# Optimization experiments

Hardware: AMD Instinct MI355X
Metric: run time of the kernel (lower is better)

## Reference

```python
import jax, jax.numpy as jnp
import numpy as np

B = 262144   # number of (group, item) prediction pairs
M = 16       # max members per group (ragged -> padded)
NU = 100000  # num_users
NI = 50000   # num_items
D = 32       # embedding_dim (hardcoded via torch.zeros([32]))


def setup_inputs() -> dict:
    key = jax.random.key(0)
    ks = jax.random.split(key, 9)
    item_inputs = jax.random.randint(ks[0], (B,), 0, NI)
    member_ids = jax.random.randint(ks[1], (B, M), 0, NU)
    lengths = jax.random.randint(ks[2], (B, 1), 1, M + 1)
    member_mask = jnp.arange(M)[None, :] < lengths  # [B, M] bool, variable group sizes
    user_table = jax.random.normal(ks[3], (NU, D), jnp.float32) * 0.1  # xavier-ish
    item_table = jax.random.normal(ks[4], (NI, D), jnp.float32) * 0.1
    W_bil = jax.random.normal(ks[5], (D, D), jnp.float32)  # nn.Bilinear(D, D, 1) weight[0]
    b_bil = jax.random.normal(ks[6], (1,), jnp.float32) * 0.05
    W1 = jax.random.normal(ks[7], (8, 3 * D), jnp.float32) * 0.05  # Linear(96, 8)
    b1 = jnp.zeros((8,), jnp.float32)
    W2 = jax.random.normal(ks[8], (1, 8), jnp.float32) * 0.05  # Linear(8, 1)
    b2 = jnp.zeros((1,), jnp.float32)
    return {
        "item_inputs": item_inputs, "member_ids": member_ids, "member_mask": member_mask,
        "user_table": user_table, "item_table": item_table,
        "W_bil": W_bil, "b_bil": b_bil, "W1": W1, "b1": b1, "W2": W2, "b2": b2,
    }


def reference(item_inputs, member_ids, member_mask, user_table, item_table,
              W_bil, b_bil, W1, b1, W2, b2):
    item_e = item_table[item_inputs]          # [B, D] gather
    mem_e = user_table[member_ids]            # [B, M, D] gather
    # bilinear attention score per member: m^T W i + b (softmax in original is computed then discarded)
    scores = jnp.einsum('bmd,de,be->bm', mem_e, W_bil, item_e) + b_bil[0]
    w = scores * member_mask.astype(scores.dtype)  # zero out padded members (ragged groups)
    final_user = jnp.einsum('bm,bmd->bd', w, mem_e)  # unnormalized weighted sum of members
    new_embeds = jnp.concatenate([final_user * item_e, final_user, item_e], axis=-1)  # [B, 3D]
    h = jax.nn.relu(new_embeds @ W1.T + b1)
    y = jax.nn.sigmoid(h @ W2.T + b2)          # [B, 1]
    return y
```

## Files before the change

kernel.cpp:

```cpp
#include <hip/hip_runtime.h>
#include <math.h>

#define DD 32
#define MM 16
#define TROW 72

__device__ __forceinline__ void load8f4(const float* __restrict__ p, float* r) {
    const float4* q = (const float4*)p;
#pragma unroll
    for (int i = 0; i < 8; ++i) {
        float4 v = q[i];
        r[4*i+0] = v.x; r[4*i+1] = v.y; r[4*i+2] = v.z; r[4*i+3] = v.w;
    }
}

__global__ void precompute_item(const float* __restrict__ item_table,
                                const float* __restrict__ W_bil,
                                const float* __restrict__ W1,
                                float* __restrict__ tbl, int NI) {
    int g = blockIdx.x * blockDim.x + threadIdx.x;
    if (g >= NI * DD) return;
    int i = g >> 5;
    int d = g & (DD - 1);
    float it[DD];
    load8f4(item_table + (size_t)i * DD, it);
    const float* w = W_bil + d * DD;
    float s0 = 0.f, s1 = 0.f, s2 = 0.f, s3 = 0.f;
#pragma unroll
    for (int e = 0; e < DD; e += 4) {
        s0 = fmaf(w[e+0], it[e+0], s0);
        s1 = fmaf(w[e+1], it[e+1], s1);
        s2 = fmaf(w[e+2], it[e+2], s2);
        s3 = fmaf(w[e+3], it[e+3], s3);
    }
    float* o = tbl + (size_t)i * TROW;
    o[d]      = (s0 + s1) + (s2 + s3);
    o[DD + d] = it[d];
    if (d < 8) {
        const float* w1 = W1 + d * 96 + 64;
        float c0 = 0.f, c1 = 0.f, c2 = 0.f, c3 = 0.f;
#pragma unroll
        for (int e = 0; e < DD; e += 4) {
            c0 = fmaf(w1[e+0], it[e+0], c0);
            c1 = fmaf(w1[e+1], it[e+1], c1);
            c2 = fmaf(w1[e+2], it[e+2], c2);
            c3 = fmaf(w1[e+3], it[e+3], c3);
        }
        o[64 + d] = (c0 + c1) + (c2 + c3);
    }
}

__device__ __forceinline__ void member1(const float* __restrict__ ut, int id,
                                        const float* __restrict__ t, float bb,
                                        float* __restrict__ fin) {
    float me[DD];
    load8f4(ut + (size_t)id * DD, me);
    float s0 = 0.f, s1 = 0.f, s2 = 0.f, s3 = 0.f;
#pragma unroll
    for (int d = 0; d < DD; d += 4) {
        s0 = fmaf(me[d+0], t[d+0], s0);
        s1 = fmaf(me[d+1], t[d+1], s1);
        s2 = fmaf(me[d+2], t[d+2], s2);
        s3 = fmaf(me[d+3], t[d+3], s3);
    }
    float s = ((s0 + s1) + (s2 + s3)) + bb;
#pragma unroll
    for (int d = 0; d < DD; ++d) fin[d] = fmaf(s, me[d], fin[d]);
}

__device__ __forceinline__ void member2(const float* __restrict__ ut, int ia, int ib,
                                        const float* __restrict__ t, float bb,
                                        float* __restrict__ fin) {
    float ma[DD], mb[DD];
    load8f4(ut + (size_t)ia * DD, ma);
    load8f4(ut + (size_t)ib * DD, mb);
    float a0 = 0.f, a1 = 0.f, a2 = 0.f, a3 = 0.f;
    float c0 = 0.f, c1 = 0.f, c2 = 0.f, c3 = 0.f;
#pragma unroll
    for (int d = 0; d < DD; d += 4) {
        a0 = fmaf(ma[d+0], t[d+0], a0);
        a1 = fmaf(ma[d+1], t[d+1], a1);
        a2 = fmaf(ma[d+2], t[d+2], a2);
        a3 = fmaf(ma[d+3], t[d+3], a3);
        c0 = fmaf(mb[d+0], t[d+0], c0);
        c1 = fmaf(mb[d+1], t[d+1], c1);
        c2 = fmaf(mb[d+2], t[d+2], c2);
        c3 = fmaf(mb[d+3], t[d+3], c3);
    }
    float sa = ((a0 + a1) + (a2 + a3)) + bb;
    float sb = ((c0 + c1) + (c2 + c3)) + bb;
#pragma unroll
    for (int d = 0; d < DD; ++d) fin[d] = fmaf(sa, ma[d], fin[d]);
#pragma unroll
    for (int d = 0; d < DD; ++d) fin[d] = fmaf(sb, mb[d], fin[d]);
}

template <bool USE_TBL>
__global__ __launch_bounds__(256)
void bilinear_main(const int* __restrict__ item_inputs,
                   const int* __restrict__ member_ids,
                   const unsigned char* __restrict__ member_mask,
                   const float* __restrict__ user_table,
                   const float* __restrict__ item_table,
                   const float* __restrict__ tbl,
                   const float* __restrict__ W_bil,
                   const float* __restrict__ b_bil,
                   const float* __restrict__ W1,
                   const float* __restrict__ b1v,
                   const float* __restrict__ W2,
                   const float* __restrict__ b2v,
                   float* __restrict__ out, int Btot) {
    int b = blockIdx.x * blockDim.x + threadIdx.x;
    if (b >= Btot) return;

    int item = item_inputs[b];

    uint4 mv = *(const uint4*)(member_mask + (size_t)b * MM);
    int len = __popc(mv.x & 0x01010101u) + __popc(mv.y & 0x01010101u) +
              __popc(mv.z & 0x01010101u) + __popc(mv.w & 0x01010101u);

    int ids[MM];
    {
        const int4* mp = (const int4*)(member_ids + (size_t)b * MM);
#pragma unroll
        for (int q = 0; q < 4; ++q) {
            int4 v = mp[q];
            ids[4*q+0] = v.x; ids[4*q+1] = v.y; ids[4*q+2] = v.z; ids[4*q+3] = v.w;
        }
    }

    float t[DD];
    const float* tb = nullptr;
    if (USE_TBL) {
        tb = tbl + (size_t)item * TROW;
        load8f4(tb, t);
    } else {
        float it0[DD];
        load8f4(item_table + (size_t)item * DD, it0);
#pragma unroll 4
        for (int d = 0; d < DD; ++d) {
            float s = 0.f;
#pragma unroll
            for (int e = 0; e < DD; ++e) s = fmaf(W_bil[d * DD + e], it0[e], s);
            t[d] = s;
        }
    }

    float bb = b_bil[0];
    float fin[DD];
#pragma unroll
    for (int d = 0; d < DD; ++d) fin[d] = 0.f;

    int m = 0;
    for (; m + 2 <= len; m += 2)
        member2(user_table, ids[m], ids[m+1], t, bb, fin);
    if (m < len)
        member1(user_table, ids[m], t, bb, fin);

    float it[DD];
    float cj[8];
    if (USE_TBL) {
        load8f4(tb + DD, it);
        float4 q0 = *(const float4*)(tb + 64);
        float4 q1 = *(const float4*)(tb + 68);
        cj[0] = q0.x; cj[1] = q0.y; cj[2] = q0.z; cj[3] = q0.w;
        cj[4] = q1.x; cj[5] = q1.y; cj[6] = q1.z; cj[7] = q1.w;
    } else {
        load8f4(item_table + (size_t)item * DD, it);
#pragma unroll
        for (int j = 0; j < 8; ++j) {
            float s = 0.f;
#pragma unroll
            for (int d = 0; d < DD; ++d) s = fmaf(W1[j * 96 + 64 + d], it[d], s);
            cj[j] = s;
        }
    }

    float h[8];
#pragma unroll
    for (int j = 0; j < 8; ++j) h[j] = cj[j] + b1v[j];
#pragma unroll
    for (int d = 0; d < DD; ++d) {
        float f = fin[d];
        float p = f * it[d];
#pragma unroll
        for (int j = 0; j < 8; ++j) {
            h[j] = fmaf(W1[j * 96 + d], p, h[j]);
            h[j] = fmaf(W1[j * 96 + 32 + d], f, h[j]);
        }
    }
    float z = b2v[0];
#pragma unroll
    for (int j = 0; j < 8; ++j) {
        float hv = h[j] > 0.f ? h[j] : 0.f;
        z = fmaf(W2[j], hv, z);
    }
    out[b] = 1.f / (1.f + __expf(-z));
}

extern "C" void kernel_launch(void* const* d_in, const int* in_sizes, int n_in,
                              void* d_out, int out_size, void* d_ws, size_t ws_size,
                              hipStream_t stream) {
    const int*           item_inputs = (const int*)d_in[0];
    const int*           member_ids  = (const int*)d_in[1];
    const unsigned char* member_mask = (const unsigned char*)d_in[2];
    const float*         user_table  = (const float*)d_in[3];
    const float*         item_table  = (const float*)d_in[4];
    const float*         W_bil       = (const float*)d_in[5];
    const float*         b_bil       = (const float*)d_in[6];
    const float*         W1          = (const float*)d_in[7];
    const float*         b1          = (const float*)d_in[8];
    const float*         W2          = (const float*)d_in[9];
    const float*         b2          = (const float*)d_in[10];
    float* out = (float*)d_out;

    int Btot = in_sizes[0];
    int NI   = in_sizes[4] / DD;

    bool use_tbl = ws_size >= (size_t)NI * TROW * sizeof(float);
    int blk = 256;
    if (use_tbl) {
        float* tbl = (float*)d_ws;
        precompute_item<<<(NI * DD + blk - 1) / blk, blk, 0, stream>>>(item_table, W_bil, W1, tbl, NI);
        bilinear_main<true><<<(Btot + blk - 1) / blk, blk, 0, stream>>>(
            item_inputs, member_ids, member_mask, user_table, item_table, tbl,
            W_bil, b_bil, W1, b1, W2, b2, out, Btot);
    } else {
        bilinear_main<false><<<(Btot + blk - 1) / blk, blk, 0, stream>>>(
            item_inputs, member_ids, member_mask, user_table, item_table, nullptr,
            W_bil, b_bil, W1, b1, W2, b2, out, Btot);
    }
}
```

Measured before the change: 167.1 us.

## Use nontemporal streaming loads/stores, pad item table rows, fully unroll member loop

The per-pair index, mask and member-id loads and the output store become nontemporal accesses so streaming data does not evict the gathered embedding tables from cache. The member loop is fully unrolled into eight guarded pair steps, which lets the compiler issue gathers early at the cost of more code and possibly more registers. The precomputed item table row is padded from 72 to 80 floats, which changes row alignment and increases its footprint slightly.

New measurement: 170.9 us. 2.3% more time.

```diff
diff --git a/kernel.cpp b/kernel.cpp
--- a/kernel.cpp
+++ b/kernel.cpp
@@ -3,7 +3,10 @@
 
 #define DD 32
 #define MM 16
-#define TROW 72
+#define TROW 80
+
+typedef int          vi4 __attribute__((ext_vector_type(4)));
+typedef unsigned int vu4 __attribute__((ext_vector_type(4)));
 
 __device__ __forceinline__ void load8f4(const float* __restrict__ p, float* r) {
     const float4* q = (const float4*)p;
@@ -22,8 +25,9 @@
     if (g >= NI * DD) return;
     int i = g >> 5;
     int d = g & (DD - 1);
+    const float* row = item_table + (size_t)i * DD;
     float it[DD];
-    load8f4(item_table + (size_t)i * DD, it);
+    load8f4(row, it);
     const float* w = W_bil + d * DD;
     float s0 = 0.f, s1 = 0.f, s2 = 0.f, s3 = 0.f;
 #pragma unroll
@@ -35,7 +39,7 @@
     }
     float* o = tbl + (size_t)i * TROW;
     o[d]      = (s0 + s1) + (s2 + s3);
-    o[DD + d] = it[d];
+    o[DD + d] = row[d];
     if (d < 8) {
         const float* w1 = W1 + d * 96 + 64;
         float c0 = 0.f, c1 = 0.f, c2 = 0.f, c3 = 0.f;
@@ -113,21 +117,22 @@
     int b = blockIdx.x * blockDim.x + threadIdx.x;
     if (b >= Btot) return;
 
-    int item = item_inputs[b];
-
-    uint4 mv = *(const uint4*)(member_mask + (size_t)b * MM);
-    int len = __popc(mv.x & 0x01010101u) + __popc(mv.y & 0x01010101u) +
-              __popc(mv.z & 0x01010101u) + __popc(mv.w & 0x01010101u);
-
+    int item = __builtin_nontemporal_load(item_inputs + b);
+
+    vu4 mv = __builtin_nontemporal_load((const vu4*)(member_mask + (size_t)b * MM));
+    int len = __popc(mv[0] & 0x01010101u) + __popc(mv[1] & 0x01010101u) +
+              __popc(mv[2] & 0x01010101u) + __popc(mv[3] & 0x01010101u);
+
+    const vi4* mp = (const vi4*)(member_ids + (size_t)b * MM);
+    vi4 q0 = __builtin_nontemporal_load(mp + 0);
+    vi4 q1 = __builtin_nontemporal_load(mp + 1);
+    vi4 q2 = __builtin_nontemporal_load(mp + 2);
+    vi4 q3 = __builtin_nontemporal_load(mp + 3);
     int ids[MM];
-    {
-        const int4* mp = (const int4*)(member_ids + (size_t)b * MM);
-#pragma unroll
-        for (int q = 0; q < 4; ++q) {
-            int4 v = mp[q];
-            ids[4*q+0] = v.x; ids[4*q+1] = v.y; ids[4*q+2] = v.z; ids[4*q+3] = v.w;
-        }
-    }
+    ids[0]=q0[0];  ids[1]=q0[1];  ids[2]=q0[2];  ids[3]=q0[3];
+    ids[4]=q1[0];  ids[5]=q1[1];  ids[6]=q1[2];  ids[7]=q1[3];
+    ids[8]=q2[0];  ids[9]=q2[1];  ids[10]=q2[2]; ids[11]=q2[3];
+    ids[12]=q3[0]; ids[13]=q3[1]; ids[14]=q3[2]; ids[15]=q3[3];
 
     float t[DD];
     const float* tb = nullptr;
@@ -151,20 +156,21 @@
 #pragma unroll
     for (int d = 0; d < DD; ++d) fin[d] = 0.f;
 
-    int m = 0;
-    for (; m + 2 <= len; m += 2)
-        member2(user_table, ids[m], ids[m+1], t, bb, fin);
-    if (m < len)
-        member1(user_table, ids[m], t, bb, fin);
+#pragma unroll
+    for (int p = 0; p < MM / 2; ++p) {
+        int m = 2 * p;
+        if (m + 1 < len)      member2(user_table, ids[m], ids[m + 1], t, bb, fin);
+        else if (m < len)     member1(user_table, ids[m], t, bb, fin);
+    }
 
     float it[DD];
     float cj[8];
     if (USE_TBL) {
         load8f4(tb + DD, it);
-        float4 q0 = *(const float4*)(tb + 64);
-        float4 q1 = *(const float4*)(tb + 68);
-        cj[0] = q0.x; cj[1] = q0.y; cj[2] = q0.z; cj[3] = q0.w;
-        cj[4] = q1.x; cj[5] = q1.y; cj[6] = q1.z; cj[7] = q1.w;
+        float4 g0 = *(const float4*)(tb + 64);
+        float4 g1 = *(const float4*)(tb + 68);
+        cj[0] = g0.x; cj[1] = g0.y; cj[2] = g0.z; cj[3] = g0.w;
+        cj[4] = g1.x; cj[5] = g1.y; cj[6] = g1.z; cj[7] = g1.w;
     } else {
         load8f4(item_table + (size_t)item * DD, it);
 #pragma unroll
@@ -182,10 +188,10 @@
 #pragma unroll
     for (int d = 0; d < DD; ++d) {
         float f = fin[d];
-        float p = f * it[d];
+        float pfi = f * it[d];
 #pragma unroll
         for (int j = 0; j < 8; ++j) {
-            h[j] = fmaf(W1[j * 96 + d], p, h[j]);
+            h[j] = fmaf(W1[j * 96 + d], pfi, h[j]);
             h[j] = fmaf(W1[j * 96 + 32 + d], f, h[j]);
         }
     }
@@ -195,7 +201,7 @@
         float hv = h[j] > 0.f ? h[j] : 0.f;
         z = fmaf(W2[j], hv, z);
     }
-    out[b] = 1.f / (1.f + __expf(-z));
+    __builtin_nontemporal_store(1.f / (1.f + __expf(-z)), out + b);
 }
 
 extern "C" void kernel_launch(void* const* d_in, const int* in_sizes, int n_in,
```
